# Kernel tuning notes

Hardware: AMD Instinct MI355X
Metric: run time of the kernel (lower is better)

Reference implementation:

```python
import jax, jax.numpy as jnp
import numpy as np

B, T, D = 4, 2048, 1024

def setup_inputs() -> dict:
    key = jax.random.key(0)
    kx, kq, kk, kv = jax.random.split(key, 4)
    return {
        "vector": jax.random.normal(kx, (B, T, D), dtype=jnp.float32),
        # original uses torch.rand -> uniform [0,1)
        "W_queries": jax.random.uniform(kq, (D, D), dtype=jnp.float32),
        "W_keys": jax.random.uniform(kk, (D, D), dtype=jnp.float32),
        "W_values": jax.random.uniform(kv, (D, D), dtype=jnp.float32),
    }

def reference(vector, W_queries, W_keys, W_values):
    b, num_token, d_out = vector.shape
    queries = vector @ W_queries          # [b, t, d]
    keys = vector @ W_keys                # [b, t, d]
    values = vector @ W_values            # [b, t, d]
    # attention_score: [b, q, k]
    scores = jnp.einsum('bqd,bkd->bqk', queries, keys)
    causal_mask = jnp.triu(jnp.ones((num_token, num_token), dtype=bool), k=1)
    scores = jnp.where(causal_mask[None, :, :], -jnp.inf, scores)
    # NOTE: original uses FLOOR division `//` by sqrt(d_k) -- faithful here.
    inv_sqrt_scale = jnp.asarray(np.sqrt(keys.shape[-1]), dtype=scores.dtype)
    weights = jnp.floor(scores / inv_sqrt_scale)
    # NOTE: original applies softmax over dim=1 (the query axis), not dim=-1.
    weights = jax.nn.softmax(weights, axis=1)
    # dropout rate is 0.0 (eval/deterministic): identity
    context = jnp.einsum('bqk,bkd->bqd', weights, values)
    return context
```

## Files before the change

kernel.cpp:

```cpp
#include <hip/hip_runtime.h>
#include <math.h>

typedef _Float16 half4 __attribute__((ext_vector_type(4)));
typedef _Float16 half8 __attribute__((ext_vector_type(8)));
typedef float f32x4 __attribute__((ext_vector_type(4)));

#define GLD16(gptr, lptr)                                                     \
    __builtin_amdgcn_global_load_lds(                                         \
        (const __attribute__((address_space(1))) unsigned int*)(gptr),        \
        (__attribute__((address_space(3))) unsigned int*)(lptr), 16, 0, 0)

#define WAIT_VM(N) asm volatile("s_waitcnt vmcnt(" #N ")" ::: "memory")
#define BARRIER()  __builtin_amdgcn_s_barrier()
#define SCHED_FENCE() __builtin_amdgcn_sched_barrier(0)

namespace {

constexpr int Bb = 4;
constexpr int Tt = 2048;
constexpr int Dd = 1024;
constexpr int BT = Bb * Tt;
constexpr int NCH = 16;

__device__ inline _Float16 f2h(float f) { return (_Float16)f; }

__global__ __launch_bounds__(256) void convert_x_kernel(
    const float* __restrict__ X, _Float16* __restrict__ Xhi, _Float16* __restrict__ Xlo)
{
    const int idx = (blockIdx.x * 256 + threadIdx.x) * 4;
    const float4 v = *(const float4*)(X + idx);
    const float a[4] = {v.x, v.y, v.z, v.w};
    half4 h, l;
#pragma unroll
    for (int i = 0; i < 4; ++i) {
        h[i] = f2h(a[i]);
        l[i] = f2h(a[i] - (float)h[i]);
    }
    *(half4*)(Xhi + idx) = h;
    *(half4*)(Xlo + idx) = l;
}

__global__ __launch_bounds__(256) void convert_wqk_kernel(
    const float* __restrict__ Wq, const float* __restrict__ Wk,
    _Float16* __restrict__ Wqh, _Float16* __restrict__ Wql,
    _Float16* __restrict__ Wkh, _Float16* __restrict__ Wkl)
{
    const int mat = blockIdx.y;
    const float* W = mat ? Wk : Wq;
    _Float16* Hh = mat ? Wkh : Wqh;
    _Float16* Ll = mat ? Wkl : Wql;
    const int idx = (blockIdx.x * 256 + threadIdx.x) * 4;
    const float4 v = *(const float4*)(W + idx);
    const float a[4] = {v.x, v.y, v.z, v.w};
    half4 h, l;
#pragma unroll
    for (int i = 0; i < 4; ++i) {
        h[i] = f2h(a[i]);
        l[i] = f2h(a[i] - (float)h[i]);
    }
    *(half4*)(Hh + idx) = h;
    *(half4*)(Ll + idx) = l;
}

__global__ __launch_bounds__(256) void convert_wv_kernel(
    const float* __restrict__ Wv, _Float16* __restrict__ WvTh)
{
    __shared__ float tile[64][65];
    const int n0 = blockIdx.x * 64, k0 = blockIdx.y * 64;
    const int tx = threadIdx.x & 63, ty = threadIdx.x >> 6;
#pragma unroll
    for (int i = 0; i < 16; ++i)
        tile[ty + i * 4][tx] = Wv[(size_t)(k0 + ty + i * 4) * Dd + n0 + tx];
    __syncthreads();
#pragma unroll
    for (int i = 0; i < 16; ++i) {
        const float v = tile[tx][ty + i * 4];
        WvTh[(size_t)(n0 + ty + i * 4) * Dd + k0 + tx] = f2h(v);
    }
}

__global__ __launch_bounds__(256) void gt_kernel(
    const _Float16* __restrict__ Wkh, const _Float16* __restrict__ Wkl,
    const _Float16* __restrict__ Wqh, const _Float16* __restrict__ Wql,
    _Float16* __restrict__ GTh, _Float16* __restrict__ GTl)
{
    __shared__ _Float16 Ahl[2][2][4][512];
    __shared__ _Float16 Bhl[2][2][4][512];

    const int n0 = blockIdx.x * 64;
    const int m0 = blockIdx.y * 64;
    const int tid = threadIdx.x;
    const int w = tid >> 6, lane = tid & 63;
    const int lr = lane & 15, lq = lane >> 4;
    const int wi = (w >> 1) * 2, wj = (w & 1) * 2;

    f32x4 acc[2][2];
#pragma unroll
    for (int i = 0; i < 2; ++i)
#pragma unroll
        for (int j = 0; j < 2; ++j)
#pragma unroll
            for (int c = 0; c < 4; ++c) acc[i][j][c] = 0.f;

    auto stage = [&](int bf, int kk) {
        const int s = w;
        const size_t ar = (size_t)(m0 + s * 16 + lr) * Dd + kk + lq * 8;
        const size_t br = (size_t)(n0 + s * 16 + lr) * Dd + kk + lq * 8;
        GLD16(Wkh + ar, &Ahl[bf][0][s][0]);
        GLD16(Wkl + ar, &Ahl[bf][1][s][0]);
        GLD16(Wqh + br, &Bhl[bf][0][s][0]);
        GLD16(Wql + br, &Bhl[bf][1][s][0]);
    };

    stage(0, 0);
    int ib = 0;
    for (int step = 0; step < 32; ++step, ib ^= 1) {
        if (step < 31) {
            stage(ib ^ 1, (step + 1) << 5);
            WAIT_VM(4);
        } else {
            WAIT_VM(0);
        }
        BARRIER();
        SCHED_FENCE();
        half8 ah[2], al[2], bh[2], bl[2];
#pragma unroll
        for (int i = 0; i < 2; ++i) {
            ah[i] = *(const half8*)&Ahl[ib][0][wi + i][lane * 8];
            al[i] = *(const half8*)&Ahl[ib][1][wi + i][lane * 8];
        }
#pragma unroll
        for (int j = 0; j < 2; ++j) {
            bh[j] = *(const half8*)&Bhl[ib][0][wj + j][lane * 8];
            bl[j] = *(const half8*)&Bhl[ib][1][wj + j][lane * 8];
        }
#pragma unroll
        for (int i = 0; i < 2; ++i)
#pragma unroll
            for (int j = 0; j < 2; ++j) {
                acc[i][j] = __builtin_amdgcn_mfma_f32_16x16x32_f16(ah[i], bh[j], acc[i][j], 0, 0, 0);
                acc[i][j] = __builtin_amdgcn_mfma_f32_16x16x32_f16(ah[i], bl[j], acc[i][j], 0, 0, 0);
                acc[i][j] = __builtin_amdgcn_mfma_f32_16x16x32_f16(al[i], bh[j], acc[i][j], 0, 0, 0);
            }
        BARRIER();
    }

#pragma unroll
    for (int i = 0; i < 2; ++i)
#pragma unroll
        for (int r = 0; r < 4; ++r) {
            const int row = m0 + (wi + i) * 16 + lq * 4 + r;
#pragma unroll
            for (int j = 0; j < 2; ++j) {
                const int col = n0 + (wj + j) * 16 + lr;
                const float v = acc[i][j][r];
                const _Float16 h = f2h(v);
                GTh[(size_t)row * Dd + col] = h;
                GTl[(size_t)row * Dd + col] = f2h(v - (float)h);
            }
        }
}

__global__ __launch_bounds__(256, 2) void tv_kernel(
    const _Float16* __restrict__ Xhi, const _Float16* __restrict__ Xlo,
    const _Float16* __restrict__ GTh, const _Float16* __restrict__ GTl,
    const _Float16* __restrict__ WvTh,
    _Float16* __restrict__ Thi, _Float16* __restrict__ Tlo,
    _Float16* __restrict__ Vrow)
{
    __shared__ _Float16 Ahl[2][2][8][512];
    __shared__ _Float16 Bhl[2][2][8][512];

    const int f  = blockIdx.x;
    const int fp = (f & 7) * 128 + (f >> 3);
    const int mb  = fp >> 4;
    const int sub = fp & 15;
    const int m0 = mb * 128;
    const int n0 = (sub & 7) * 128;

    const int tid = threadIdx.x;
    const int w = tid >> 6, lane = tid & 63;
    const int lr = lane & 15, lq = lane >> 4;
    const int wr = (w >> 1) * 4, wc = (w & 1) * 4;

    f32x4 acc[4][4];
#pragma unroll
    for (int i = 0; i < 4; ++i)
#pragma unroll
        for (int j = 0; j < 4; ++j)
#pragma unroll
            for (int c = 0; c < 4; ++c) acc[i][j][c] = 0.f;

    if (sub < 8) {
        auto stage = [&](int bf, int kk) {
#pragma unroll
            for (int s2 = 0; s2 < 2; ++s2) {
                const int s = w * 2 + s2;
                const size_t ar = (size_t)(m0 + s * 16 + lr) * Dd + kk + lq * 8;
                const size_t br = (size_t)(n0 + s * 16 + lr) * Dd + kk + lq * 8;
                GLD16(Xhi + ar, &Ahl[bf][0][s][0]);
                GLD16(Xlo + ar, &Ahl[bf][1][s][0]);
                GLD16(GTh + br, &Bhl[bf][0][s][0]);
                GLD16(GTl + br, &Bhl[bf][1][s][0]);
            }
        };
        stage(0, 0);
        int ib = 0;
        for (int step = 0; step < 32; ++step, ib ^= 1) {
            if (step < 31) {
                stage(ib ^ 1, (step + 1) << 5);
                WAIT_VM(8);
            } else {
                WAIT_VM(0);
            }
            BARRIER();
            SCHED_FENCE();
            half8 ah[4], al[4], bh[4], bl[4];
#pragma unroll
            for (int i = 0; i < 4; ++i) {
                ah[i] = *(const half8*)&Ahl[ib][0][wr + i][lane * 8];
                al[i] = *(const half8*)&Ahl[ib][1][wr + i][lane * 8];
            }
#pragma unroll
            for (int j = 0; j < 4; ++j) {
                bh[j] = *(const half8*)&Bhl[ib][0][wc + j][lane * 8];
                bl[j] = *(const half8*)&Bhl[ib][1][wc + j][lane * 8];
            }
#pragma unroll
            for (int i = 0; i < 4; ++i)
#pragma unroll
                for (int j = 0; j < 4; ++j) {
                    acc[i][j] = __builtin_amdgcn_mfma_f32_16x16x32_f16(ah[i], bh[j], acc[i][j], 0, 0, 0);
                    acc[i][j] = __builtin_amdgcn_mfma_f32_16x16x32_f16(ah[i], bl[j], acc[i][j], 0, 0, 0);
                    acc[i][j] = __builtin_amdgcn_mfma_f32_16x16x32_f16(al[i], bh[j], acc[i][j], 0, 0, 0);
                }
            BARRIER();
        }
#pragma unroll
        for (int i = 0; i < 4; ++i)
#pragma unroll
            for (int r = 0; r < 4; ++r) {
                const int row = m0 + (wr + i) * 16 + lq * 4 + r;
#pragma unroll
                for (int j = 0; j < 4; ++j) {
                    const int col = n0 + (wc + j) * 16 + lr;
                    const float v = acc[i][j][r];
                    const _Float16 h = f2h(v);
                    Thi[(size_t)row * Dd + col] = h;
                    Tlo[(size_t)row * Dd + col] = f2h(v - (float)h);
                }
            }
    } else {
        auto stage = [&](int bf, int kk) {
#pragma unroll
            for (int s2 = 0; s2 < 2; ++s2) {
                const int s = w * 2 + s2;
                GLD16(Xhi + (size_t)(m0 + s * 16 + lr) * Dd + kk + lq * 8, &Ahl[bf][0][s][0]);
                GLD16(WvTh + (size_t)(n0 + s * 16 + lr) * Dd + kk + lq * 8, &Bhl[bf][0][s][0]);
            }
        };
        stage(0, 0);
        int ib = 0;
        for (int step = 0; step < 32; ++step, ib ^= 1) {
            if (step < 31) {
                stage(ib ^ 1, (step + 1) << 5);
                WAIT_VM(4);
            } else {
                WAIT_VM(0);
            }
            BARRIER();
            SCHED_FENCE();
            half8 a[4], b2[4];
#pragma unroll
            for (int i = 0; i < 4; ++i) a[i] = *(const half8*)&Ahl[ib][0][wr + i][lane * 8];
#pragma unroll
            for (int j = 0; j < 4; ++j) b2[j] = *(const half8*)&Bhl[ib][0][wc + j][lane * 8];
#pragma unroll
            for (int i = 0; i < 4; ++i)
#pragma unroll
                for (int j = 0; j < 4; ++j)
                    acc[i][j] = __builtin_amdgcn_mfma_f32_16x16x32_f16(a[i], b2[j], acc[i][j], 0, 0, 0);
            BARRIER();
        }
#pragma unroll
        for (int i = 0; i < 4; ++i)
#pragma unroll
            for (int r = 0; r < 4; ++r) {
                const int row = m0 + (wr + i) * 16 + lq * 4 + r;
#pragma unroll
                for (int j = 0; j < 4; ++j)
                    Vrow[(size_t)row * Dd + n0 + (wc + j) * 16 + lr] = f2h(acc[i][j][r]);
            }
    }
}

__global__ __launch_bounds__(256) void transpose_v_kernel(
    const _Float16* __restrict__ Vrow, const float* __restrict__ Lb,
    _Float16* __restrict__ Vt)
{
    __shared__ _Float16 tile[64][78];
    const int d0 = blockIdx.x * 64, t0 = blockIdx.y * 64, b = blockIdx.z;
    const int tx = threadIdx.x & 63, ty = threadIdx.x >> 6;
#pragma unroll
    for (int i = 0; i < 16; ++i)
        tile[ty + i * 4][tx] = Vrow[((size_t)b * Tt + t0 + ty + i * 4) * Dd + d0 + tx];
    __syncthreads();
    const float sc = Lb[(size_t)b * Tt + t0 + tx];
#pragma unroll
    for (int i = 0; i < 16; ++i) {
        const float v = (float)tile[tx][ty + i * 4] * sc;
        Vt[(size_t)b * Dd * Tt + (size_t)(d0 + ty + i * 4) * Tt + t0 + tx] = f2h(v);
    }
}

__global__ __launch_bounds__(256, 2) void scores_mfma_kernel(
    const _Float16* __restrict__ Thi, const _Float16* __restrict__ Tlo,
    const _Float16* __restrict__ Xhi, const _Float16* __restrict__ Xlo,
    float* __restrict__ S, float* __restrict__ Pm, float* __restrict__ Pl)
{
    const int f  = blockIdx.x;
    const int fp = (f & 7) * 68 + (f >> 3);
    const int b = fp / 136;
    const int t = fp - b * 136;
    int byi = (int)((sqrtf(8.f * t + 1.f) - 1.f) * 0.5f);
    if ((byi + 1) * (byi + 2) / 2 <= t) ++byi;
    if (byi * (byi + 1) / 2 > t) --byi;
    const int bxi = t - byi * (byi + 1) / 2;
    const int j0 = bxi * 128, q0 = byi * 128;
    float* Sb = S + (size_t)b * Tt * Tt;

    __shared__ _Float16 Ahl[2][2][8][512];
    __shared__ _Float16 Bhl[2][2][8][512];
    const _Float16* Th = Thi + (size_t)b * Tt * Dd;
    const _Float16* Tl = Tlo + (size_t)b * Tt * Dd;
    const _Float16* Xh = Xhi + (size_t)b * Tt * Dd;
    const _Float16* Xl = Xlo + (size_t)b * Tt * Dd;

    const int tid = threadIdx.x;
    const int w = tid >> 6, lane = tid & 63;
    const int lr = lane & 15, lq = lane >> 4;
    const int wr = (w >> 1) * 4, wc = (w & 1) * 4;

    f32x4 acc[4][4];
#pragma unroll
    for (int i = 0; i < 4; ++i)
#pragma unroll
        for (int j = 0; j < 4; ++j)
#pragma unroll
            for (int c = 0; c < 4; ++c) acc[i][j][c] = 0.f;

    auto stage = [&](int bf, int kk) {
#pragma unroll
        for (int s2 = 0; s2 < 2; ++s2) {
            const int s = w * 2 + s2;
            const size_t ar = (size_t)(q0 + s * 16 + lr) * Dd + kk + lq * 8;
            const size_t br = (size_t)(j0 + s * 16 + lr) * Dd + kk + lq * 8;
            GLD16(Th + ar, &Ahl[bf][0][s][0]);
            GLD16(Tl + ar, &Ahl[bf][1][s][0]);
            GLD16(Xh + br, &Bhl[bf][0][s][0]);
            GLD16(Xl + br, &Bhl[bf][1][s][0]);
        }
    };

    stage(0, 0);
    int ib = 0;
    for (int step = 0; step < 32; ++step, ib ^= 1) {
        if (step < 31) {
            stage(ib ^ 1, (step + 1) << 5);
            WAIT_VM(8);
        } else {
            WAIT_VM(0);
        }
        BARRIER();
        SCHED_FENCE();
        half8 ah[4], al[4], bh[4], bl[4];
#pragma unroll
        for (int i = 0; i < 4; ++i) {
            ah[i] = *(const half8*)&Ahl[ib][0][wr + i][lane * 8];
            al[i] = *(const half8*)&Ahl[ib][1][wr + i][lane * 8];
        }
#pragma unroll
        for (int j = 0; j < 4; ++j) {
            bh[j] = *(const half8*)&Bhl[ib][0][wc + j][lane * 8];
            bl[j] = *(const half8*)&Bhl[ib][1][wc + j][lane * 8];
        }
#pragma unroll
        for (int i = 0; i < 4; ++i)
#pragma unroll
            for (int j = 0; j < 4; ++j) {
                acc[i][j] = __builtin_amdgcn_mfma_f32_16x16x32_f16(ah[i], bh[j], acc[i][j], 0, 0, 0);
                acc[i][j] = __builtin_amdgcn_mfma_f32_16x16x32_f16(ah[i], bl[j], acc[i][j], 0, 0, 0);
                acc[i][j] = __builtin_amdgcn_mfma_f32_16x16x32_f16(al[i], bh[j], acc[i][j], 0, 0, 0);
            }
        BARRIER();
    }

    float sv[4][4][4];
#pragma unroll
    for (int i = 0; i < 4; ++i)
#pragma unroll
        for (int r = 0; r < 4; ++r) {
            const int q = q0 + (wr + i) * 16 + lq * 4 + r;
#pragma unroll
            for (int j = 0; j < 4; ++j) {
                const int jg = j0 + (wc + j) * 16 + lr;
                const float v = (jg <= q) ? floorf(acc[i][j][r] * 0.03125f) : -INFINITY;
                sv[i][j][r] = v;
                Sb[(size_t)q * Tt + jg] = v;
            }
        }

    float* red  = (float*)&Ahl[0][0][0][0];
    float* colm = red + 2048;
    __syncthreads();
    for (int e = tid; e < 2048; e += 256) red[e] = -INFINITY;
    __syncthreads();
    const int rowidx = (w * 4 + lq) * 128;
#pragma unroll
    for (int j = 0; j < 4; ++j) {
        const int c = (wc + j) * 16 + lr;
        float lm = -INFINITY;
#pragma unroll
        for (int i = 0; i < 4; ++i)
#pragma unroll
            for (int r = 0; r < 4; ++r) lm = fmaxf(lm, sv[i][j][r]);
        red[rowidx + c] = lm;
    }
    __syncthreads();
    if (tid < 128) {
        float m = -INFINITY;
#pragma unroll
        for (int e = 0; e < 16; ++e) m = fmaxf(m, red[e * 128 + tid]);
        colm[tid] = m;
    }
    __syncthreads();
    float ls[4];
#pragma unroll
    for (int j = 0; j < 4; ++j) {
        const int c = (wc + j) * 16 + lr;
        const float m = colm[c];
        float s = 0.f;
#pragma unroll
        for (int i = 0; i < 4; ++i)
#pragma unroll
            for (int r = 0; r < 4; ++r)
                if (sv[i][j][r] != -INFINITY) s += __expf(sv[i][j][r] - m);
        ls[j] = s;
    }
    __syncthreads();
    for (int e = tid; e < 2048; e += 256) red[e] = 0.f;
    __syncthreads();
#pragma unroll
    for (int j = 0; j < 4; ++j) red[rowidx + (wc + j) * 16 + lr] = ls[j];
    __syncthreads();
    if (tid < 128) {
        float l = 0.f;
#pragma unroll
        for (int e = 0; e < 16; ++e) l += red[e * 128 + tid];
        const size_t o = ((size_t)b * NCH + byi) * Tt + j0 + tid;
        Pm[o] = colm[tid];
        Pl[o] = l;
    }
}

__global__ __launch_bounds__(256) void colstats_merge_kernel(
    const float* __restrict__ Pm, const float* __restrict__ Pl,
    float* __restrict__ Mb, float* __restrict__ Lb)
{
    const int j = blockIdx.x * 256 + threadIdx.x;
    const int b = blockIdx.y;
    const int jt = j >> 7;
    float m = -INFINITY, l = 0.f;
    for (int c = jt; c < NCH; ++c) {
        const size_t pidx = ((size_t)b * NCH + c) * Tt + j;
        const float mi = Pm[pidx];
        if (mi == -INFINITY) continue;
        const float li = Pl[pidx];
        if (mi > m) { l = l * __expf(m - mi) + li; m = mi; }
        else        { l += li * __expf(mi - m); }
    }
    Mb[(size_t)b * Tt + j] = m;
    Lb[(size_t)b * Tt + j] = (l > 0.f) ? 1.f / l : 0.f;
}

__global__ __launch_bounds__(256) void pmat_kernel(
    const float* __restrict__ S, const float* __restrict__ Mb,
    _Float16* __restrict__ P)
{
    const int t = blockIdx.x;
    int byi = (int)((sqrtf(8.f * t + 1.f) - 1.f) * 0.5f);
    if ((byi + 1) * (byi + 2) / 2 <= t) ++byi;
    if (byi * (byi + 1) / 2 > t) --byi;
    const int bxi = t - byi * (byi + 1) / 2;
    const int b = blockIdx.z;
    const int j0 = bxi * 128, q0 = byi * 128;

    const int tr = threadIdx.x >> 4;
    const int tc = (threadIdx.x & 15) * 8;
    const float* mp = Mb + (size_t)b * Tt + j0 + tc;
    float mv[8];
#pragma unroll
    for (int e = 0; e < 8; ++e) mv[e] = mp[e];

#pragma unroll
    for (int it = 0; it < 8; ++it) {
        const int row = q0 + it * 16 + tr;
        const float* Sp = S + (size_t)b * Tt * Tt + (size_t)row * Tt + j0 + tc;
        const float4 s0 = *(const float4*)Sp;
        const float4 s1 = *(const float4*)(Sp + 4);
        const float sa[8] = {s0.x, s0.y, s0.z, s0.w, s1.x, s1.y, s1.z, s1.w};
        half8 out;
#pragma unroll
        for (int e = 0; e < 8; ++e) {
            const int jg = j0 + tc + e;
            out[e] = (jg <= row) ? f2h(__expf(sa[e] - mv[e])) : (_Float16)0.f;
        }
        *(half8*)(P + (size_t)b * Tt * Tt + (size_t)row * Tt + j0 + tc) = out;
    }
}

__global__ __launch_bounds__(256) void context_mfma_kernel(
    const _Float16* __restrict__ P, const _Float16* __restrict__ Vt,
    float* __restrict__ Out)
{
    __shared__ _Float16 Al[2][8][512];
    __shared__ _Float16 Bl[2][8][512];

    const int f  = blockIdx.x;
    const int fp = (f & 7) * 64 + (f >> 3);
    const int b  = fp >> 7;
    const int r  = fp & 127;
    const int bx = r & 7;
    const int tq = r >> 3;
    const int by = (tq & 1) ? (15 - (tq >> 1)) : (tq >> 1);
    const int d0 = bx * 128;
    const int q0 = by * 128;
    const _Float16* Pb = P + (size_t)b * Tt * Tt;
    const _Float16* Vb = Vt + (size_t)b * Dd * Tt;
    float* Ob = Out + (size_t)b * Tt * Dd;

    const int tid = threadIdx.x;
    const int w = tid >> 6, lane = tid & 63;
    const int lr = lane & 15, lq = lane >> 4;
    const int wr = (w >> 1) * 4, wc = (w & 1) * 4;

    f32x4 acc[4][4];
#pragma unroll
    for (int i = 0; i < 4; ++i)
#pragma unroll
        for (int j = 0; j < 4; ++j)
#pragma unroll
            for (int c = 0; c < 4; ++c) acc[i][j][c] = 0.f;

    auto stage = [&](int bf, int k0) {
#pragma unroll
        for (int s2 = 0; s2 < 2; ++s2) {
            const int s = w * 2 + s2;
            GLD16(Pb + (size_t)(q0 + s * 16 + lr) * Tt + k0 + lq * 8, &Al[bf][s][0]);
            GLD16(Vb + (size_t)(d0 + s * 16 + lr) * Tt + k0 + lq * 8, &Bl[bf][s][0]);
        }
    };

    const int nstep = (q0 + 128) >> 5;
    stage(0, 0);
    int ib = 0;
    for (int step = 0; step < nstep; ++step, ib ^= 1) {
        if (step + 1 < nstep) {
            stage(ib ^ 1, (step + 1) << 5);
            WAIT_VM(4);
        } else {
            WAIT_VM(0);
        }
        BARRIER();
        SCHED_FENCE();
        half8 a[4], b2[4];
#pragma unroll
        for (int i = 0; i < 4; ++i) a[i] = *(const half8*)&Al[ib][wr + i][lane * 8];
#pragma unroll
        for (int j = 0; j < 4; ++j) b2[j] = *(const half8*)&Bl[ib][wc + j][lane * 8];
#pragma unroll
        for (int i = 0; i < 4; ++i)
#pragma unroll
            for (int j = 0; j < 4; ++j)
                acc[i][j] = __builtin_amdgcn_mfma_f32_16x16x32_f16(a[i], b2[j], acc[i][j], 0, 0, 0);
        BARRIER();
    }

#pragma unroll
    for (int i = 0; i < 4; ++i)
#pragma unroll
        for (int r2 = 0; r2 < 4; ++r2) {
            const int row = q0 + (wr + i) * 16 + lq * 4 + r2;
#pragma unroll
            for (int j = 0; j < 4; ++j)
                Ob[(size_t)row * Dd + d0 + (wc + j) * 16 + lr] = acc[i][j][r2];
        }
}

}

extern "C" void kernel_launch(void* const* d_in, const int* in_sizes, int n_in,
                              void* d_out, int out_size, void* d_ws, size_t ws_size,
                              hipStream_t stream)
{
    const float* X  = (const float*)d_in[0];
    const float* Wq = (const float*)d_in[1];
    const float* Wk = (const float*)d_in[2];
    const float* Wv = (const float*)d_in[3];

    char* ws = (char*)d_ws;
    const size_t MB = 1024 * 1024;
    _Float16* Xhi  = (_Float16*)ws;
    _Float16* Xlo  = (_Float16*)(ws + 16 * MB);
    _Float16* Wqh  = (_Float16*)(ws + 32 * MB);
    _Float16* Wql  = (_Float16*)(ws + 34 * MB);
    _Float16* Wkh  = (_Float16*)(ws + 36 * MB);
    _Float16* Wkl  = (_Float16*)(ws + 38 * MB);
    _Float16* WvTh = (_Float16*)(ws + 40 * MB);
    _Float16* GTh  = (_Float16*)(ws + 44 * MB);
    _Float16* GTl  = (_Float16*)(ws + 46 * MB);
    _Float16* Thi  = (_Float16*)(ws + 48 * MB);
    _Float16* Tlo  = (_Float16*)(ws + 64 * MB);
    _Float16* P    = Thi;
    _Float16* Vt   = (_Float16*)(ws + 80 * MB);
    _Float16* Vrow = (_Float16*)(ws + 96 * MB);
    float*    S    = (float*)(ws + 112 * MB);
    float*    Mb   = (float*)(ws + 176 * MB);
    float*    Lb   = Mb + (size_t)Bb * Tt;
    float*    Pm   = Lb + (size_t)Bb * Tt;
    float*    Pl   = Pm + (size_t)Bb * NCH * Tt;
    float*    Out  = (float*)d_out;

    convert_x_kernel<<<BT * Dd / 1024, 256, 0, stream>>>(X, Xhi, Xlo);
    convert_wqk_kernel<<<dim3(Dd * Dd / 1024, 2), 256, 0, stream>>>(Wq, Wk, Wqh, Wql, Wkh, Wkl);
    convert_wv_kernel<<<dim3(16, 16), 256, 0, stream>>>(Wv, WvTh);
    gt_kernel<<<dim3(16, 16), 256, 0, stream>>>(Wkh, Wkl, Wqh, Wql, GTh, GTl);
    tv_kernel<<<dim3(1024), 256, 0, stream>>>(Xhi, Xlo, GTh, GTl, WvTh, Thi, Tlo, Vrow);
    scores_mfma_kernel<<<dim3(544), 256, 0, stream>>>(Thi, Tlo, Xhi, Xlo, S, Pm, Pl);
    colstats_merge_kernel<<<dim3(Tt / 256, Bb), 256, 0, stream>>>(Pm, Pl, Mb, Lb);
    transpose_v_kernel<<<dim3(Dd / 64, Tt / 64, Bb), 256, 0, stream>>>(Vrow, Lb, Vt);
    pmat_kernel<<<dim3(136, 1, Bb), 256, 0, stream>>>(S, Mb, P);
    context_mfma_kernel<<<dim3(512), 256, 0, stream>>>(P, Vt, Out);
}
```

Baseline: 452.0 us.

## Fuse V transpose into tv epilogue and softmax exponent into context GEMM

The tv kernel now transposes its V tile through shared memory and writes Vt directly, which removes the separate transpose kernel and the Vrow round trip. The pmat kernel is gone. The context GEMM now loads fp32 scores, computes exp(s - m) * (1/l) in registers and stores the fp16 A tile to LDS, so the P matrix is never materialised. The trade-off is that each of the 8 d-column blocks re-reads and re-exponentiates the same fp32 score tiles. The A operand also loses double buffering and gains extra block-wide syncs, and causal masking now relies on S already holding masked values.

```diff
diff --git a/kernel.cpp b/kernel.cpp
--- a/kernel.cpp
+++ b/kernel.cpp
@@ -166,10 +166,15 @@
     const _Float16* __restrict__ GTh, const _Float16* __restrict__ GTl,
     const _Float16* __restrict__ WvTh,
     _Float16* __restrict__ Thi, _Float16* __restrict__ Tlo,
-    _Float16* __restrict__ Vrow)
-{
-    __shared__ _Float16 Ahl[2][2][8][512];
-    __shared__ _Float16 Bhl[2][2][8][512];
+    _Float16* __restrict__ Vt)
+{
+    __shared__ _Float16 smem[32768];
+    auto A_ = [&](int bf, int hl, int s) -> _Float16* {
+        return smem + ((bf * 2 + hl) * 8 + s) * 512;
+    };
+    auto B_ = [&](int bf, int hl, int s) -> _Float16* {
+        return smem + 16384 + ((bf * 2 + hl) * 8 + s) * 512;
+    };
 
     const int f  = blockIdx.x;
     const int fp = (f & 7) * 128 + (f >> 3);
@@ -198,10 +203,10 @@
                 const int s = w * 2 + s2;
                 const size_t ar = (size_t)(m0 + s * 16 + lr) * Dd + kk + lq * 8;
                 const size_t br = (size_t)(n0 + s * 16 + lr) * Dd + kk + lq * 8;
-                GLD16(Xhi + ar, &Ahl[bf][0][s][0]);
-                GLD16(Xlo + ar, &Ahl[bf][1][s][0]);
-                GLD16(GTh + br, &Bhl[bf][0][s][0]);
-                GLD16(GTl + br, &Bhl[bf][1][s][0]);
+                GLD16(Xhi + ar, A_(bf, 0, s));
+                GLD16(Xlo + ar, A_(bf, 1, s));
+                GLD16(GTh + br, B_(bf, 0, s));
+                GLD16(GTl + br, B_(bf, 1, s));
             }
         };
         stage(0, 0);
@@ -218,13 +223,13 @@
             half8 ah[4], al[4], bh[4], bl[4];
 #pragma unroll
             for (int i = 0; i < 4; ++i) {
-                ah[i] = *(const half8*)&Ahl[ib][0][wr + i][lane * 8];
-                al[i] = *(const half8*)&Ahl[ib][1][wr + i][lane * 8];
+                ah[i] = *(const half8*)(A_(ib, 0, wr + i) + lane * 8);
+                al[i] = *(const half8*)(A_(ib, 1, wr + i) + lane * 8);
             }
 #pragma unroll
             for (int j = 0; j < 4; ++j) {
-                bh[j] = *(const half8*)&Bhl[ib][0][wc + j][lane * 8];
-                bl[j] = *(const half8*)&Bhl[ib][1][wc + j][lane * 8];
+                bh[j] = *(const half8*)(B_(ib, 0, wc + j) + lane * 8);
+                bl[j] = *(const half8*)(B_(ib, 1, wc + j) + lane * 8);
             }
 #pragma unroll
             for (int i = 0; i < 4; ++i)
@@ -255,8 +260,8 @@
 #pragma unroll
             for (int s2 = 0; s2 < 2; ++s2) {
                 const int s = w * 2 + s2;
-                GLD16(Xhi + (size_t)(m0 + s * 16 + lr) * Dd + kk + lq * 8, &Ahl[bf][0][s][0]);
-                GLD16(WvTh + (size_t)(n0 + s * 16 + lr) * Dd + kk + lq * 8, &Bhl[bf][0][s][0]);
+                GLD16(Xhi + (size_t)(m0 + s * 16 + lr) * Dd + kk + lq * 8, A_(bf, 0, s));
+                GLD16(WvTh + (size_t)(n0 + s * 16 + lr) * Dd + kk + lq * 8, B_(bf, 0, s));
             }
         };
         stage(0, 0);
@@ -272,9 +277,9 @@
             SCHED_FENCE();
             half8 a[4], b2[4];
 #pragma unroll
-            for (int i = 0; i < 4; ++i) a[i] = *(const half8*)&Ahl[ib][0][wr + i][lane * 8];
-#pragma unroll
-            for (int j = 0; j < 4; ++j) b2[j] = *(const half8*)&Bhl[ib][0][wc + j][lane * 8];
+            for (int i = 0; i < 4; ++i) a[i] = *(const half8*)(A_(ib, 0, wr + i) + lane * 8);
+#pragma unroll
+            for (int j = 0; j < 4; ++j) b2[j] = *(const half8*)(B_(ib, 0, wc + j) + lane * 8);
 #pragma unroll
             for (int i = 0; i < 4; ++i)
 #pragma unroll
@@ -282,34 +287,26 @@
                     acc[i][j] = __builtin_amdgcn_mfma_f32_16x16x32_f16(a[i], b2[j], acc[i][j], 0, 0, 0);
             BARRIER();
         }
+        __syncthreads();
 #pragma unroll
         for (int i = 0; i < 4; ++i)
 #pragma unroll
-            for (int r = 0; r < 4; ++r) {
-                const int row = m0 + (wr + i) * 16 + lq * 4 + r;
-#pragma unroll
-                for (int j = 0; j < 4; ++j)
-                    Vrow[(size_t)row * Dd + n0 + (wc + j) * 16 + lr] = f2h(acc[i][j][r]);
-            }
-    }
-}
-
-__global__ __launch_bounds__(256) void transpose_v_kernel(
-    const _Float16* __restrict__ Vrow, const float* __restrict__ Lb,
-    _Float16* __restrict__ Vt)
-{
-    __shared__ _Float16 tile[64][78];
-    const int d0 = blockIdx.x * 64, t0 = blockIdx.y * 64, b = blockIdx.z;
-    const int tx = threadIdx.x & 63, ty = threadIdx.x >> 6;
-#pragma unroll
-    for (int i = 0; i < 16; ++i)
-        tile[ty + i * 4][tx] = Vrow[((size_t)b * Tt + t0 + ty + i * 4) * Dd + d0 + tx];
-    __syncthreads();
-    const float sc = Lb[(size_t)b * Tt + t0 + tx];
-#pragma unroll
-    for (int i = 0; i < 16; ++i) {
-        const float v = (float)tile[tx][ty + i * 4] * sc;
-        Vt[(size_t)b * Dd * Tt + (size_t)(d0 + ty + i * 4) * Tt + t0 + tx] = f2h(v);
+            for (int r2 = 0; r2 < 4; ++r2) {
+                const int rloc = (wr + i) * 16 + lq * 4 + r2;
+#pragma unroll
+                for (int j = 0; j < 4; ++j) {
+                    const int cloc = (wc + j) * 16 + lr;
+                    smem[cloc * 136 + rloc] = f2h(acc[i][j][r2]);
+                }
+            }
+        __syncthreads();
+        const int b2i = m0 >> 11;
+        const int t0  = m0 & 2047;
+        const int dloc = tid >> 1, tl = (tid & 1) * 64;
+        _Float16* vp = Vt + (size_t)b2i * Dd * Tt + (size_t)(n0 + dloc) * Tt + t0 + tl;
+#pragma unroll
+        for (int e = 0; e < 8; ++e)
+            *(half8*)(vp + e * 8) = *(const half8*)&smem[dloc * 136 + tl + e * 8];
     }
 }
 
@@ -483,47 +480,12 @@
     Lb[(size_t)b * Tt + j] = (l > 0.f) ? 1.f / l : 0.f;
 }
 
-__global__ __launch_bounds__(256) void pmat_kernel(
+__global__ __launch_bounds__(256) void context_mfma_kernel(
     const float* __restrict__ S, const float* __restrict__ Mb,
-    _Float16* __restrict__ P)
-{
-    const int t = blockIdx.x;
-    int byi = (int)((sqrtf(8.f * t + 1.f) - 1.f) * 0.5f);
-    if ((byi + 1) * (byi + 2) / 2 <= t) ++byi;
-    if (byi * (byi + 1) / 2 > t) --byi;
-    const int bxi = t - byi * (byi + 1) / 2;
-    const int b = blockIdx.z;
-    const int j0 = bxi * 128, q0 = byi * 128;
-
-    const int tr = threadIdx.x >> 4;
-    const int tc = (threadIdx.x & 15) * 8;
-    const float* mp = Mb + (size_t)b * Tt + j0 + tc;
-    float mv[8];
-#pragma unroll
-    for (int e = 0; e < 8; ++e) mv[e] = mp[e];
-
-#pragma unroll
-    for (int it = 0; it < 8; ++it) {
-        const int row = q0 + it * 16 + tr;
-        const float* Sp = S + (size_t)b * Tt * Tt + (size_t)row * Tt + j0 + tc;
-        const float4 s0 = *(const float4*)Sp;
-        const float4 s1 = *(const float4*)(Sp + 4);
-        const float sa[8] = {s0.x, s0.y, s0.z, s0.w, s1.x, s1.y, s1.z, s1.w};
-        half8 out;
-#pragma unroll
-        for (int e = 0; e < 8; ++e) {
-            const int jg = j0 + tc + e;
-            out[e] = (jg <= row) ? f2h(__expf(sa[e] - mv[e])) : (_Float16)0.f;
-        }
-        *(half8*)(P + (size_t)b * Tt * Tt + (size_t)row * Tt + j0 + tc) = out;
-    }
-}
-
-__global__ __launch_bounds__(256) void context_mfma_kernel(
-    const _Float16* __restrict__ P, const _Float16* __restrict__ Vt,
+    const float* __restrict__ Lb, const _Float16* __restrict__ Vt,
     float* __restrict__ Out)
 {
-    __shared__ _Float16 Al[2][8][512];
+    __shared__ _Float16 As[8][512];
     __shared__ _Float16 Bl[2][8][512];
 
     const int f  = blockIdx.x;
@@ -535,7 +497,9 @@
     const int by = (tq & 1) ? (15 - (tq >> 1)) : (tq >> 1);
     const int d0 = bx * 128;
     const int q0 = by * 128;
-    const _Float16* Pb = P + (size_t)b * Tt * Tt;
+    const float* Sb = S + (size_t)b * Tt * Tt;
+    const float* Mp = Mb + (size_t)b * Tt;
+    const float* Lp = Lb + (size_t)b * Tt;
     const _Float16* Vb = Vt + (size_t)b * Dd * Tt;
     float* Ob = Out + (size_t)b * Tt * Dd;
 
@@ -552,30 +516,57 @@
 #pragma unroll
             for (int c = 0; c < 4; ++c) acc[i][j][c] = 0.f;
 
-    auto stage = [&](int bf, int k0) {
+    float4 sreg[4];
+    float4 mreg[2], lreg[2];
+
+    auto issue = [&](int ib2, int k0) {
+        const int kc = k0 + lq * 8;
 #pragma unroll
         for (int s2 = 0; s2 < 2; ++s2) {
             const int s = w * 2 + s2;
-            GLD16(Pb + (size_t)(q0 + s * 16 + lr) * Tt + k0 + lq * 8, &Al[bf][s][0]);
-            GLD16(Vb + (size_t)(d0 + s * 16 + lr) * Tt + k0 + lq * 8, &Bl[bf][s][0]);
+            const float* sp = Sb + (size_t)(q0 + s * 16 + lr) * Tt + kc;
+            sreg[s2 * 2]     = *(const float4*)sp;
+            sreg[s2 * 2 + 1] = *(const float4*)(sp + 4);
+        }
+        mreg[0] = *(const float4*)(Mp + kc);
+        mreg[1] = *(const float4*)(Mp + kc + 4);
+        lreg[0] = *(const float4*)(Lp + kc);
+        lreg[1] = *(const float4*)(Lp + kc + 4);
+#pragma unroll
+        for (int s2 = 0; s2 < 2; ++s2) {
+            const int s = w * 2 + s2;
+            GLD16(Vb + (size_t)(d0 + s * 16 + lr) * Tt + k0 + lq * 8, &Bl[ib2][s][0]);
         }
     };
+    auto writeA = [&]() {
+        const float mm[8] = {mreg[0].x, mreg[0].y, mreg[0].z, mreg[0].w,
+                             mreg[1].x, mreg[1].y, mreg[1].z, mreg[1].w};
+        const float ll[8] = {lreg[0].x, lreg[0].y, lreg[0].z, lreg[0].w,
+                             lreg[1].x, lreg[1].y, lreg[1].z, lreg[1].w};
+#pragma unroll
+        for (int s2 = 0; s2 < 2; ++s2) {
+            const int s = w * 2 + s2;
+            const float4 s0 = sreg[s2 * 2], s1 = sreg[s2 * 2 + 1];
+            const float sa[8] = {s0.x, s0.y, s0.z, s0.w, s1.x, s1.y, s1.z, s1.w};
+            half8 out;
+#pragma unroll
+            for (int e = 0; e < 8; ++e)
+                out[e] = f2h(__expf(sa[e] - mm[e]) * ll[e]);
+            *(half8*)&As[s][lane * 8] = out;
+        }
+    };
 
     const int nstep = (q0 + 128) >> 5;
-    stage(0, 0);
+    issue(0, 0);
+    writeA();
+    __syncthreads();
     int ib = 0;
     for (int step = 0; step < nstep; ++step, ib ^= 1) {
-        if (step + 1 < nstep) {
-            stage(ib ^ 1, (step + 1) << 5);
-            WAIT_VM(4);
-        } else {
-            WAIT_VM(0);
-        }
-        BARRIER();
-        SCHED_FENCE();
+        const bool more = (step + 1 < nstep);
+        if (more) issue(ib ^ 1, (step + 1) << 5);
         half8 a[4], b2[4];
 #pragma unroll
-        for (int i = 0; i < 4; ++i) a[i] = *(const half8*)&Al[ib][wr + i][lane * 8];
+        for (int i = 0; i < 4; ++i) a[i] = *(const half8*)&As[wr + i][lane * 8];
 #pragma unroll
         for (int j = 0; j < 4; ++j) b2[j] = *(const half8*)&Bl[ib][wc + j][lane * 8];
 #pragma unroll
@@ -583,7 +574,11 @@
 #pragma unroll
             for (int j = 0; j < 4; ++j)
                 acc[i][j] = __builtin_amdgcn_mfma_f32_16x16x32_f16(a[i], b2[j], acc[i][j], 0, 0, 0);
-        BARRIER();
+        if (more) {
+            __syncthreads();
+            writeA();
+            __syncthreads();
+        }
     }
 
 #pragma unroll
@@ -621,9 +616,7 @@
     _Float16* GTl  = (_Float16*)(ws + 46 * MB);
     _Float16* Thi  = (_Float16*)(ws + 48 * MB);
     _Float16* Tlo  = (_Float16*)(ws + 64 * MB);
-    _Float16* P    = Thi;
     _Float16* Vt   = (_Float16*)(ws + 80 * MB);
-    _Float16* Vrow = (_Float16*)(ws + 96 * MB);
     float*    S    = (float*)(ws + 112 * MB);
     float*    Mb   = (float*)(ws + 176 * MB);
     float*    Lb   = Mb + (size_t)Bb * Tt;
@@ -635,10 +628,8 @@
     convert_wqk_kernel<<<dim3(Dd * Dd / 1024, 2), 256, 0, stream>>>(Wq, Wk, Wqh, Wql, Wkh, Wkl);
     convert_wv_kernel<<<dim3(16, 16), 256, 0, stream>>>(Wv, WvTh);
     gt_kernel<<<dim3(16, 16), 256, 0, stream>>>(Wkh, Wkl, Wqh, Wql, GTh, GTl);
-    tv_kernel<<<dim3(1024), 256, 0, stream>>>(Xhi, Xlo, GTh, GTl, WvTh, Thi, Tlo, Vrow);
+    tv_kernel<<<dim3(1024), 256, 0, stream>>>(Xhi, Xlo, GTh, GTl, WvTh, Thi, Tlo, Vt);
     scores_mfma_kernel<<<dim3(544), 256, 0, stream>>>(Thi, Tlo, Xhi, Xlo, S, Pm, Pl);
     colstats_merge_kernel<<<dim3(Tt / 256, Bb), 256, 0, stream>>>(Pm, Pl, Mb, Lb);
-    transpose_v_kernel<<<dim3(Dd / 64, Tt / 64, Bb), 256, 0, stream>>>(Vrow, Lb, Vt);
-    pmat_kernel<<<dim3(136, 1, Bb), 256, 0, stream>>>(S, Mb, P);
-    context_mfma_kernel<<<dim3(512), 256, 0, stream>>>(P, Vt, Out);
-}
+    context_mfma_kernel<<<dim3(512), 256, 0, stream>>>(S, Mb, Lb, Vt, Out);
+}
```

Measured after the change: 469.7 us. 1.04x slower.
